# Performance work log

Measured on AMD Instinct MI355X. Metric: run time of the kernel, lower is better.

Reference implementation:

```python
import jax, jax.numpy as jnp
import numpy as np

H = 16          # num_heads
RMS_EPS = 1.1920928955078125e-07  # torch.finfo(float32).eps (F.rms_norm default)
NORM_EPS = 1e-12                  # F.normalize default eps


def _rms_norm(t):
    # F.rms_norm without weight: t / sqrt(mean(t^2) + eps)
    ms = jnp.mean(t * t, axis=-1, keepdims=True)
    return t * jax.lax.rsqrt(ms + RMS_EPS)


def setup_inputs() -> dict:
    key = jax.random.key(0)
    k1, k2, k3 = jax.random.split(key, 3)
    B, N, C = 2, 2048, 1024
    x = jax.random.normal(k1, (B, N, C), dtype=jnp.float32)
    # nn.Linear weights are (out_features, in_features); scale like kaiming-uniform-ish
    w_qkv = jax.random.normal(k2, (3 * C, C), dtype=jnp.float32) * (C ** -0.5)
    w_proj = jax.random.normal(k3, (C, C), dtype=jnp.float32) * (C ** -0.5)
    return {"x": x, "w_qkv": w_qkv, "w_proj": w_proj}


def reference(x, w_qkv, w_proj):
    B, N, C = x.shape
    D = C // H
    scale = D ** -0.5
    qkv = x @ w_qkv.T                                  # (B,N,3C)
    qkv = qkv.reshape(B, N, 3, H, D)
    q = qkv[:, :, 0].transpose(0, 2, 1, 3)             # (B,H,N,D)
    k = qkv[:, :, 1].transpose(0, 2, 1, 3)
    v = qkv[:, :, 2].transpose(0, 2, 1, 3)
    q = _rms_norm(q)
    k = _rms_norm(k)
    attn = jnp.einsum('bhnd,bhmd->bhnm', q, k) * scale  # (B,H,N,N)
    attn = jax.nn.softmax(attn, axis=-1)
    y = jnp.einsum('bhnm,bhmd->bhnd', attn, v)          # (B,H,N,D)
    # xsa: subtract projection of y onto normalized v
    vnorm = jnp.linalg.norm(v, axis=-1, keepdims=True)
    Vn = v / jnp.maximum(vnorm, NORM_EPS)
    y = y - jnp.sum(y * Vn, axis=-1, keepdims=True) * Vn
    out = y.transpose(0, 2, 1, 3).reshape(B, N, C)
    return out @ w_proj.T
```

## Files before the change

kernel.cpp:

```cpp
#include <hip/hip_runtime.h>
#include <hip/hip_bf16.h>
#include <cstdint>

#define RMS_EPS 1.1920928955078125e-07f

typedef __bf16 bf16;
typedef __attribute__((ext_vector_type(8))) __bf16 bf16x8;
typedef __attribute__((ext_vector_type(4))) __bf16 bf16x4;
typedef __attribute__((ext_vector_type(4))) float f32x4;
typedef __attribute__((ext_vector_type(16))) float f32x16;
typedef unsigned int u32;
typedef __attribute__((ext_vector_type(4))) u32 u32x4;

__device__ __forceinline__ void gload16(const bf16* g, bf16* l) {
  __builtin_amdgcn_global_load_lds(
      (__attribute__((address_space(1))) void*)(g),
      (__attribute__((address_space(3))) void*)(l), 16, 0, 0);
}

__device__ __forceinline__ float fexp2(float x) {
#if __has_builtin(__builtin_amdgcn_exp2f)
  return __builtin_amdgcn_exp2f(x);
#else
  return exp2f(x);
#endif
}

__device__ __forceinline__ u32 pack2(float a, float b) {
  unsigned short xa = __builtin_bit_cast(unsigned short, (bf16)a);
  unsigned short xb = __builtin_bit_cast(unsigned short, (bf16)b);
  return (u32)xa | ((u32)xb << 16);
}

__global__ __launch_bounds__(256) void cvt3_kernel(
    const float* __restrict__ x, const float* __restrict__ wq, const float* __restrict__ wp,
    bf16* __restrict__ xo, bf16* __restrict__ wqo, bf16* __restrict__ wpo) {
  int i = blockIdx.x * 256 + threadIdx.x;
  const float* s; bf16* d; int off;
  if (i < 524288) { s = x; d = xo; off = i; }
  else if (i < 917504) { s = wq; d = wqo; off = i - 524288; }
  else { s = wp; d = wpo; off = i - 917504; }
  const float4* s4 = (const float4*)s;
  float4 a = s4[off * 2], b = s4[off * 2 + 1];
  bf16x8 o;
  o[0] = (bf16)a.x; o[1] = (bf16)a.y; o[2] = (bf16)a.z; o[3] = (bf16)a.w;
  o[4] = (bf16)b.x; o[5] = (bf16)b.y; o[6] = (bf16)b.z; o[7] = (bf16)b.w;
  *(bf16x8*)(d + off * 8) = o;
}

template <int MODE>
__global__ __launch_bounds__(256, 2) void gemm_bt(
    const bf16* __restrict__ A, const bf16* __restrict__ B,
    float* __restrict__ Cout, int Ncols,
    bf16* __restrict__ Qb, bf16* __restrict__ Kb, bf16* __restrict__ VtG,
    float* __restrict__ vninv) {
  __shared__ bf16 As[128 * 64];
  __shared__ bf16 Bs[128 * 64];
  const int tid = threadIdx.x;
  const int wave = tid >> 6, lane = tid & 63;
  const int l15 = lane & 15, g = lane >> 4;
  const int nwg = gridDim.x * gridDim.y;
  const int wg0 = blockIdx.y * gridDim.x + blockIdx.x;
  const int wg = (wg0 & 7) * (nwg >> 3) + (wg0 >> 3);
  const int m0 = (wg / gridDim.x) * 128, n0 = (wg % gridDim.x) * 128;
  const int wr = wave >> 1, wc = wave & 1;

  f32x4 acc[4][4] = {};

  for (int k0 = 0; k0 < 1024; k0 += 64) {
    __syncthreads();
#pragma unroll
    for (int i = 0; i < 4; ++i) {
      const int gid = (i * 4 + wave) * 64 + lane;
      const int row = gid >> 3, gk = gid & 7;
      const int srcoff = k0 + ((gk ^ (row & 7)) << 3);
      gload16(A + (m0 + row) * 1024 + srcoff, As + (i * 4 + wave) * 512);
      gload16(B + (n0 + row) * 1024 + srcoff, Bs + (i * 4 + wave) * 512);
    }
    __syncthreads();
#pragma unroll
    for (int kc = 0; kc < 2; ++kc) {
      bf16x8 af[4], bfb[4];
#pragma unroll
      for (int mi = 0; mi < 4; ++mi) {
        const int row = wr * 64 + mi * 16 + l15;
        af[mi] = *(const bf16x8*)&As[row * 64 + (((kc * 4 + g) ^ (l15 & 7)) << 3)];
      }
#pragma unroll
      for (int ni = 0; ni < 4; ++ni) {
        const int row = wc * 64 + ni * 16 + l15;
        bfb[ni] = *(const bf16x8*)&Bs[row * 64 + (((kc * 4 + g) ^ (l15 & 7)) << 3)];
      }
#pragma unroll
      for (int mi = 0; mi < 4; ++mi)
#pragma unroll
        for (int ni = 0; ni < 4; ++ni)
          acc[mi][ni] = __builtin_amdgcn_mfma_f32_16x16x32_bf16(af[mi], bfb[ni], acc[mi][ni], 0, 0, 0);
    }
  }

  if (MODE == 0) {
#pragma unroll
    for (int mi = 0; mi < 4; ++mi) {
      const int mrow = m0 + wr * 64 + mi * 16 + g * 4;
#pragma unroll
      for (int r = 0; r < 4; ++r) {
        float* cp = Cout + (long)(mrow + r) * Ncols + n0 + wc * 64 + l15;
#pragma unroll
        for (int ni = 0; ni < 4; ++ni) cp[ni * 16] = acc[mi][ni][r];
      }
    }
  } else {
    const int ncol = n0 + wc * 64;
    const int which = ncol >> 10;
    const int h = (ncol >> 6) & 15;
#pragma unroll
    for (int mi = 0; mi < 4; ++mi) {
#pragma unroll
      for (int r = 0; r < 4; ++r) {
        float ss = 0.f;
#pragma unroll
        for (int ni = 0; ni < 4; ++ni) ss += acc[mi][ni][r] * acc[mi][ni][r];
        ss += __shfl_xor(ss, 1); ss += __shfl_xor(ss, 2);
        ss += __shfl_xor(ss, 4); ss += __shfl_xor(ss, 8);
        const int m = m0 + wr * 64 + mi * 16 + g * 4 + r;
        const int b = m >> 11, nseq = m & 2047;
        const int bh = b * 16 + h;
        const long base = ((long)bh * 2048 + nseq) * 64 + l15;
        if (which == 0) {
          const float sc = rsqrtf(ss * (1.0f / 64) + RMS_EPS) * (0.125f * 1.44269504088896340736f);
#pragma unroll
          for (int ni = 0; ni < 4; ++ni) Qb[base + ni * 16] = (bf16)(acc[mi][ni][r] * sc);
        } else if (which == 1) {
          const float sc = rsqrtf(ss * (1.0f / 64) + RMS_EPS);
#pragma unroll
          for (int ni = 0; ni < 4; ++ni) Kb[base + ni * 16] = (bf16)(acc[mi][ni][r] * sc);
        } else {
          const long vbase = (long)bh * 64 * 2048 + nseq;
#pragma unroll
          for (int ni = 0; ni < 4; ++ni)
            VtG[vbase + (long)(ni * 16 + l15) * 2048] = (bf16)acc[mi][ni][r];
          if (l15 == 0) vninv[bh * 2048 + nseq] = 1.0f / fmaxf(sqrtf(ss), 1e-12f);
        }
      }
    }
  }
}

__global__ __launch_bounds__(256, 2) void attn_kernel(
    const bf16* __restrict__ Qb, const bf16* __restrict__ Kb, const bf16* __restrict__ VtG,
    const float* __restrict__ vninv, bf16* __restrict__ Yb) {
  __shared__ bf16 Ks[2][64 * 64];
  __shared__ bf16 Vt[2][64 * 64];

  const int tid = threadIdx.x;
  const int wq = tid >> 6;
  const int lane = tid & 63;
  const int l31 = lane & 31, hi = lane >> 5;
  const int wg = (blockIdx.x & 7) * (gridDim.x >> 3) + (blockIdx.x >> 3);
  const int bh = wg >> 4, qb = wg & 15;
  const int b = bh >> 4, h = bh & 15;
  const long off = (long)bh * (2048 * 64);
  const bf16* Qp = Qb + off;
  const bf16* Kp = Kb + off;
  const bf16* VtP = VtG + (long)bh * 64 * 2048;
  const int qrow = qb * 128 + wq * 32 + l31;

  bf16x8 qf[4];
#pragma unroll
  for (int kc = 0; kc < 4; ++kc)
    qf[kc] = *(const bf16x8*)&Qp[qrow * 64 + kc * 16 + hi * 8];

  f32x16 o[2] = {};
  float mrun = -__builtin_inff();
  float lrun = 0.f;

  const int kj = lane >> 3, kgk = lane & 7;
  int koff[2], voff[2];
#pragma unroll
  for (int i = 0; i < 2; ++i) {
    const int chunk = i * 4 + wq;
    const int row = chunk * 8 + kj;
    const int sw = (kgk ^ (row & 7)) << 3;
    koff[i] = row * 64 + sw;
    voff[i] = row * 2048 + sw;
  }

#pragma unroll
  for (int i = 0; i < 2; ++i) {
    const int chunk = i * 4 + wq;
    gload16(Kp + koff[i], &Ks[0][chunk * 512]);
    gload16(VtP + voff[i], &Vt[0][chunk * 512]);
  }
  __syncthreads();

  int cur = 0;
  for (int kv0 = 0; kv0 < 2048; kv0 += 64) {
    if (kv0 + 64 < 2048) {
#pragma unroll
      for (int i = 0; i < 2; ++i) {
        const int chunk = i * 4 + wq;
        gload16(Kp + (kv0 + 64) * 64 + koff[i], &Ks[cur ^ 1][chunk * 512]);
        gload16(VtP + (kv0 + 64) + voff[i], &Vt[cur ^ 1][chunk * 512]);
      }
    }
    const bf16* ks = &Ks[cur][0];
    const bf16* vt = &Vt[cur][0];

    f32x16 sv[2] = {};
    __builtin_amdgcn_s_setprio(1);
#pragma unroll
    for (int jt = 0; jt < 2; ++jt) {
      const int j = jt * 32 + l31;
#pragma unroll
      for (int kc = 0; kc < 4; ++kc) {
        bf16x8 kf = *(const bf16x8*)&ks[j * 64 + (((2 * kc + hi) ^ (j & 7)) << 3)];
        sv[jt] = __builtin_amdgcn_mfma_f32_32x32x16_bf16(kf, qf[kc], sv[jt], 0, 0, 0);
      }
    }
    __builtin_amdgcn_s_setprio(0);

    float mx[16];
#pragma unroll
    for (int r = 0; r < 16; ++r) mx[r] = fmaxf(sv[0][r], sv[1][r]);
#pragma unroll
    for (int s2 = 8; s2 > 0; s2 >>= 1)
#pragma unroll
      for (int r = 0; r < s2; ++r) mx[r] = fmaxf(mx[r], mx[r + s2]);
    float pmax = fmaxf(mx[0], __shfl_xor(mx[0], 32));

    if (!__all(pmax <= mrun + 8.f)) {
      const float mn = fmaxf(mrun, pmax);
      const float al = fexp2(mrun - mn);
      mrun = mn;
      lrun *= al;
#pragma unroll
      for (int dt = 0; dt < 2; ++dt)
#pragma unroll
        for (int r = 0; r < 16; ++r) o[dt][r] *= al;
    }

#pragma unroll
    for (int jt = 0; jt < 2; ++jt)
#pragma unroll
      for (int r = 0; r < 16; ++r) sv[jt][r] = fexp2(sv[jt][r] - mrun);
    float sm[16];
#pragma unroll
    for (int r = 0; r < 16; ++r) sm[r] = sv[0][r] + sv[1][r];
#pragma unroll
    for (int s2 = 8; s2 > 0; s2 >>= 1)
#pragma unroll
      for (int r = 0; r < s2; ++r) sm[r] += sm[r + s2];
    lrun += sm[0] + __shfl_xor(sm[0], 32);

    u32 w[2][8], pw[2][8];
#pragma unroll
    for (int jt = 0; jt < 2; ++jt)
#pragma unroll
      for (int i = 0; i < 8; ++i) {
        w[jt][i] = pack2(sv[jt][2 * i], sv[jt][2 * i + 1]);
        pw[jt][i] = __shfl_xor(w[jt][i], 32);
      }
    bf16x8 pafr[4];
#pragma unroll
    for (int kc = 0; kc < 4; ++kc) {
      const int c = kc & 1, jt = kc >> 1;
      u32x4 pv;
      pv[0] = hi ? pw[jt][4 * c + 2] : w[jt][4 * c];
      pv[1] = hi ? pw[jt][4 * c + 3] : w[jt][4 * c + 1];
      pv[2] = hi ? w[jt][4 * c + 2] : pw[jt][4 * c];
      pv[3] = hi ? w[jt][4 * c + 3] : pw[jt][4 * c + 1];
      pafr[kc] = __builtin_bit_cast(bf16x8, pv);
    }

    __builtin_amdgcn_s_setprio(1);
#pragma unroll
    for (int dt = 0; dt < 2; ++dt) {
      const int d = dt * 32 + l31;
#pragma unroll
      for (int kc = 0; kc < 4; ++kc) {
        bf16x8 vf = *(const bf16x8*)&vt[d * 64 + (((2 * kc + hi) ^ (l31 & 7)) << 3)];
        o[dt] = __builtin_amdgcn_mfma_f32_32x32x16_bf16(vf, pafr[kc], o[dt], 0, 0, 0);
      }
    }
    __builtin_amdgcn_s_setprio(0);

    __syncthreads();
    cur ^= 1;
  }

  const float linv = 1.f / lrun;
  const float vni = vninv[bh * 2048 + qrow];
  const float cvn = vni * vni;
  const bf16* vq = VtP + qrow;
  float yv[2][16], vvf[2][16];
  float t = 0.f;
#pragma unroll
  for (int dt = 0; dt < 2; ++dt)
#pragma unroll
    for (int rr = 0; rr < 4; ++rr) {
#pragma unroll
      for (int e = 0; e < 4; ++e) {
        const int r = rr * 4 + e;
        const int d = e + 8 * rr + 4 * hi + 32 * dt;
        const float y = o[dt][r] * linv;
        const float vx = (float)vq[d * 2048];
        yv[dt][r] = y; vvf[dt][r] = vx;
        t += y * vx;
      }
    }
  t += __shfl_xor(t, 32);
  const float coef = t * cvn;
  bf16* yp = Yb + ((long)b * 2048 + qrow) * 1024 + h * 64;
#pragma unroll
  for (int dt = 0; dt < 2; ++dt)
#pragma unroll
    for (int rr = 0; rr < 4; ++rr) {
      bf16x4 y4;
#pragma unroll
      for (int e = 0; e < 4; ++e) {
        const int r = rr * 4 + e;
        y4[e] = (bf16)(yv[dt][r] - coef * vvf[dt][r]);
      }
      *(bf16x4*)&yp[dt * 32 + rr * 8 + hi * 4] = y4;
    }
}

extern "C" void kernel_launch(void* const* d_in, const int* in_sizes, int n_in,
                              void* d_out, int out_size, void* d_ws, size_t ws_size,
                              hipStream_t stream) {
  (void)in_sizes; (void)n_in; (void)out_size; (void)ws_size;
  const float* x = (const float*)d_in[0];
  const float* w_qkv = (const float*)d_in[1];
  const float* w_proj = (const float*)d_in[2];
  float* out = (float*)d_out;
  char* ws = (char*)d_ws;

  bf16* xb     = (bf16*)(ws);
  bf16* wqkvb  = (bf16*)(ws + 8388608);
  bf16* wprojb = (bf16*)(ws + 14680064);
  bf16* Qb     = (bf16*)(ws + 16777216);
  bf16* Kb     = (bf16*)(ws + 25165824);
  bf16* VtG    = (bf16*)(ws + 33554432);
  float* vninv = (float*)(ws + 41943040);
  bf16* Yb     = (bf16*)(ws + 42467328);

  cvt3_kernel<<<4096, 256, 0, stream>>>(x, w_qkv, w_proj, xb, wqkvb, wprojb);

  gemm_bt<1><<<dim3(24, 32), 256, 0, stream>>>(xb, wqkvb, nullptr, 3072,
                                               Qb, Kb, VtG, vninv);
  attn_kernel<<<512, 256, 0, stream>>>(Qb, Kb, VtG, vninv, Yb);
  gemm_bt<0><<<dim3(8, 32), 256, 0, stream>>>(Yb, wprojb, out, 1024,
                                              nullptr, nullptr, nullptr, nullptr);
}
```

Measured before the change: 142.3 us.

## Double KV tile to 128 keys per iteration with new LDS swizzle

The flash-attention inner loop now processes 128 keys per iteration instead of 64, so per-tile softmax bookkeeping (max/sum reductions, rescale checks, barriers) is amortized over twice the MFMA work. LDS buffers are doubled to hold 128-key K and V^T tiles, and the XOR swizzle is changed to mix higher row bits to avoid bank conflicts with the new layout. The P-fragment permutation is reworked to shuffle only the needed halves, halving cross-lane shuffles. This raises LDS use (64KB per block) and register pressure, which may threaten the 2-blocks-per-CU occupancy target.

```diff
diff --git a/kernel.cpp b/kernel.cpp
--- a/kernel.cpp
+++ b/kernel.cpp
@@ -150,8 +150,8 @@
 __global__ __launch_bounds__(256, 2) void attn_kernel(
     const bf16* __restrict__ Qb, const bf16* __restrict__ Kb, const bf16* __restrict__ VtG,
     const float* __restrict__ vninv, bf16* __restrict__ Yb) {
-  __shared__ bf16 Ks[2][64 * 64];
-  __shared__ bf16 Vt[2][64 * 64];
+  __shared__ bf16 Ks[2][128 * 64];
+  __shared__ bf16 Vt[2][64 * 128];
 
   const int tid = threadIdx.x;
   const int wq = tid >> 6;
@@ -175,19 +175,18 @@
   float mrun = -__builtin_inff();
   float lrun = 0.f;
 
-  const int kj = lane >> 3, kgk = lane & 7;
-  int koff[2], voff[2];
-#pragma unroll
-  for (int i = 0; i < 2; ++i) {
+  int koff[4], voff[4];
+#pragma unroll
+  for (int i = 0; i < 4; ++i) {
     const int chunk = i * 4 + wq;
-    const int row = chunk * 8 + kj;
-    const int sw = (kgk ^ (row & 7)) << 3;
-    koff[i] = row * 64 + sw;
-    voff[i] = row * 2048 + sw;
-  }
-
-#pragma unroll
-  for (int i = 0; i < 2; ++i) {
+    const int j = chunk * 8 + (lane >> 3);
+    koff[i] = j * 64 + (((lane & 7) ^ ((j ^ (j >> 3)) & 7)) << 3);
+    const int d = chunk * 4 + (lane >> 4);
+    voff[i] = d * 2048 + (((lane & 15) ^ ((d ^ (d >> 3)) & 7)) << 3);
+  }
+
+#pragma unroll
+  for (int i = 0; i < 4; ++i) {
     const int chunk = i * 4 + wq;
     gload16(Kp + koff[i], &Ks[0][chunk * 512]);
     gload16(VtP + voff[i], &Vt[0][chunk * 512]);
@@ -195,26 +194,28 @@
   __syncthreads();
 
   int cur = 0;
-  for (int kv0 = 0; kv0 < 2048; kv0 += 64) {
-    if (kv0 + 64 < 2048) {
-#pragma unroll
-      for (int i = 0; i < 2; ++i) {
+  for (int it = 0; it < 16; ++it) {
+    const int kv0 = it * 128;
+    if (it < 15) {
+#pragma unroll
+      for (int i = 0; i < 4; ++i) {
         const int chunk = i * 4 + wq;
-        gload16(Kp + (kv0 + 64) * 64 + koff[i], &Ks[cur ^ 1][chunk * 512]);
-        gload16(VtP + (kv0 + 64) + voff[i], &Vt[cur ^ 1][chunk * 512]);
+        gload16(Kp + (kv0 + 128) * 64 + koff[i], &Ks[cur ^ 1][chunk * 512]);
+        gload16(VtP + (kv0 + 128) + voff[i], &Vt[cur ^ 1][chunk * 512]);
       }
     }
     const bf16* ks = &Ks[cur][0];
     const bf16* vt = &Vt[cur][0];
 
-    f32x16 sv[2] = {};
+    f32x16 sv[4] = {};
     __builtin_amdgcn_s_setprio(1);
 #pragma unroll
-    for (int jt = 0; jt < 2; ++jt) {
+    for (int jt = 0; jt < 4; ++jt) {
       const int j = jt * 32 + l31;
+      const int key = (j ^ (j >> 3)) & 7;
 #pragma unroll
       for (int kc = 0; kc < 4; ++kc) {
-        bf16x8 kf = *(const bf16x8*)&ks[j * 64 + (((2 * kc + hi) ^ (j & 7)) << 3)];
+        bf16x8 kf = *(const bf16x8*)&ks[j * 64 + (((2 * kc + hi) ^ key) << 3)];
         sv[jt] = __builtin_amdgcn_mfma_f32_32x32x16_bf16(kf, qf[kc], sv[jt], 0, 0, 0);
       }
     }
@@ -222,7 +223,8 @@
 
     float mx[16];
 #pragma unroll
-    for (int r = 0; r < 16; ++r) mx[r] = fmaxf(sv[0][r], sv[1][r]);
+    for (int r = 0; r < 16; ++r)
+      mx[r] = fmaxf(fmaxf(sv[0][r], sv[1][r]), fmaxf(sv[2][r], sv[3][r]));
 #pragma unroll
     for (int s2 = 8; s2 > 0; s2 >>= 1)
 #pragma unroll
@@ -241,35 +243,37 @@
     }
 
 #pragma unroll
-    for (int jt = 0; jt < 2; ++jt)
+    for (int jt = 0; jt < 4; ++jt)
 #pragma unroll
       for (int r = 0; r < 16; ++r) sv[jt][r] = fexp2(sv[jt][r] - mrun);
     float sm[16];
 #pragma unroll
-    for (int r = 0; r < 16; ++r) sm[r] = sv[0][r] + sv[1][r];
+    for (int r = 0; r < 16; ++r)
+      sm[r] = (sv[0][r] + sv[1][r]) + (sv[2][r] + sv[3][r]);
 #pragma unroll
     for (int s2 = 8; s2 > 0; s2 >>= 1)
 #pragma unroll
       for (int r = 0; r < s2; ++r) sm[r] += sm[r + s2];
     lrun += sm[0] + __shfl_xor(sm[0], 32);
 
-    u32 w[2][8], pw[2][8];
-#pragma unroll
-    for (int jt = 0; jt < 2; ++jt)
-#pragma unroll
-      for (int i = 0; i < 8; ++i) {
-        w[jt][i] = pack2(sv[jt][2 * i], sv[jt][2 * i + 1]);
-        pw[jt][i] = __shfl_xor(w[jt][i], 32);
-      }
-    bf16x8 pafr[4];
-#pragma unroll
-    for (int kc = 0; kc < 4; ++kc) {
+    u32 w[4][8];
+#pragma unroll
+    for (int jt = 0; jt < 4; ++jt)
+#pragma unroll
+      for (int i = 0; i < 8; ++i) w[jt][i] = pack2(sv[jt][2 * i], sv[jt][2 * i + 1]);
+    bf16x8 pafr[8];
+#pragma unroll
+    for (int kc = 0; kc < 8; ++kc) {
       const int c = kc & 1, jt = kc >> 1;
+      const u32 z1 = hi ? w[jt][4 * c + 0] : w[jt][4 * c + 2];
+      const u32 z2 = hi ? w[jt][4 * c + 1] : w[jt][4 * c + 3];
+      const u32 r1 = __shfl_xor(z1, 32);
+      const u32 r2 = __shfl_xor(z2, 32);
       u32x4 pv;
-      pv[0] = hi ? pw[jt][4 * c + 2] : w[jt][4 * c];
-      pv[1] = hi ? pw[jt][4 * c + 3] : w[jt][4 * c + 1];
-      pv[2] = hi ? w[jt][4 * c + 2] : pw[jt][4 * c];
-      pv[3] = hi ? w[jt][4 * c + 3] : pw[jt][4 * c + 1];
+      pv[0] = hi ? r1 : w[jt][4 * c + 0];
+      pv[1] = hi ? r2 : w[jt][4 * c + 1];
+      pv[2] = hi ? w[jt][4 * c + 2] : r1;
+      pv[3] = hi ? w[jt][4 * c + 3] : r2;
       pafr[kc] = __builtin_bit_cast(bf16x8, pv);
     }
 
@@ -277,9 +281,10 @@
 #pragma unroll
     for (int dt = 0; dt < 2; ++dt) {
       const int d = dt * 32 + l31;
-#pragma unroll
-      for (int kc = 0; kc < 4; ++kc) {
-        bf16x8 vf = *(const bf16x8*)&vt[d * 64 + (((2 * kc + hi) ^ (l31 & 7)) << 3)];
+      const int key = (d ^ (d >> 3)) & 7;
+#pragma unroll
+      for (int kc = 0; kc < 8; ++kc) {
+        bf16x8 vf = *(const bf16x8*)&vt[d * 128 + (((2 * kc + hi) ^ key) << 3)];
         o[dt] = __builtin_amdgcn_mfma_f32_32x32x16_bf16(vf, pafr[kc], o[dt], 0, 0, 0);
       }
     }
```

After: 133.8 us. 6.0% less time.
